# Kernel tuning notes

Measured on AMD Instinct MI355X. Metric: run time of the kernel, lower is better.

Reference implementation:

```python
import jax, jax.numpy as jnp
import numpy as np

DIM = 2048
N_HEADS = 32
HEAD_DIM = DIM // N_HEADS
D_FF = 4 * DIM
EPS = 1e-5


def layernorm(x, g, b):
    mu = jnp.mean(x, axis=-1, keepdims=True)
    var = jnp.mean(jnp.square(x - mu), axis=-1, keepdims=True)
    return (x - mu) * jax.lax.rsqrt(var + EPS) * g + b


def setup_inputs() -> dict:
    key = jax.random.key(0)
    ks = jax.random.split(key, 12)
    s = 0.02
    # Linear weights stored as [in, out] (y = x @ W + b), equivalent math to torch's x @ W.T
    return {
        "x": jax.random.normal(ks[0], (2, 2048, DIM), jnp.float32),
        "w_qkv": jax.random.normal(ks[1], (DIM, 3 * DIM), jnp.float32) * s,
        "b_qkv": jnp.zeros((3 * DIM,), jnp.float32),
        "w_o": jax.random.normal(ks[2], (DIM, DIM), jnp.float32) * s,
        "b_o": jnp.zeros((DIM,), jnp.float32),
        "g1": jnp.ones((DIM,), jnp.float32),
        "beta1": jnp.zeros((DIM,), jnp.float32),
        "w1": jax.random.normal(ks[3], (DIM, D_FF), jnp.float32) * s,
        "b1": jnp.zeros((D_FF,), jnp.float32),
        "w2": jax.random.normal(ks[4], (D_FF, DIM), jnp.float32) * s,
        "b2": jnp.zeros((DIM,), jnp.float32),
        "g2": jnp.ones((DIM,), jnp.float32),
        "beta2": jnp.zeros((DIM,), jnp.float32),
    }


def reference(x, w_qkv, b_qkv, w_o, b_o, g1, beta1, w1, b1, w2, b2, g2, beta2):
    B, T, _ = x.shape
    residual = x
    h = layernorm(x, g1, beta1)
    qkv = h @ w_qkv + b_qkv                      # [B,T,3*DIM]
    qkv = qkv.reshape(B, T, 3, N_HEADS, HEAD_DIM)
    qkv = jnp.transpose(qkv, (2, 0, 3, 1, 4))    # [3,B,H,T,D]
    q, k, v = qkv[0], qkv[1], qkv[2]
    scores = jnp.einsum("bhtd,bhsd->bhts", q, k) / np.sqrt(HEAD_DIM).astype(np.float32)
    attn = jax.nn.softmax(scores, axis=-1)       # full T x T (non-causal), as in source
    out = jnp.einsum("bhts,bhsd->bhtd", attn, v)
    out = jnp.transpose(out, (0, 2, 1, 3)).reshape(B, T, DIM)
    h = out @ w_o + b_o
    x = h + residual
    residual = x
    h = layernorm(x, g2, beta2)
    h = jax.nn.gelu(h @ w1 + b1, approximate=False)  # torch nn.GELU default = exact erf
    h = h @ w2 + b2
    return h + residual
```

## Files before the change

kernel.cpp:

```cpp
#include <hip/hip_runtime.h>
#include <hip/hip_bf16.h>

#define DIM  2048
#define DFF  8192
#define NH   32
#define HD   64
#define TT   2048
#define MM   4096

typedef __attribute__((ext_vector_type(4))) float f32x4;
typedef __attribute__((ext_vector_type(4))) unsigned int u32x4;
typedef __attribute__((ext_vector_type(2))) unsigned int u32x2;
typedef unsigned short ushort_t;

#define MFMA16(ACC, A, B) \
  asm volatile("v_mfma_f32_16x16x32_bf16 %0, %1, %2, %0" : "+v"(ACC) : "v"(A), "v"(B))
#define MFMA16A(ACC, A, B) \
  asm volatile("v_mfma_f32_16x16x32_bf16 %0, %1, %2, %0" : "+a"(ACC) : "v"(A), "v"(B))

#define GL16(GP, LP)                                                     \
  __builtin_amdgcn_global_load_lds(                                      \
      (const __attribute__((address_space(1))) void*)(GP),               \
      (__attribute__((address_space(3))) void*)(LP), 16, 0, 0)

#define VM(N) asm volatile("s_waitcnt vmcnt(" #N ")" ::: "memory")
#define NOOP  ((void)0)

template <int IMM>
__device__ __forceinline__ u32x4 dsr(unsigned a) {
  u32x4 d;
  asm volatile("ds_read_b128 %0, %1 offset:%2" : "=v"(d) : "v"(a), "i"(IMM));
  return d;
}

__device__ __forceinline__ unsigned int f2bu(float f) {
  union { __hip_bfloat16 h; unsigned short u; } c;
  c.h = __float2bfloat16(f);
  return (unsigned int)c.u;
}

__global__ __launch_bounds__(256)
void transpose_cvt(const float* __restrict__ in, __hip_bfloat16* __restrict__ out,
                   int R, int C) {
  __shared__ float tile[32][33];
  const int tx = threadIdx.x, ty = threadIdx.y;
  const int bx = blockIdx.x * 32, by = blockIdx.y * 32;
#pragma unroll
  for (int i = 0; i < 32; i += 8)
    tile[ty + i][tx] = in[(size_t)(by + ty + i) * C + bx + tx];
  __syncthreads();
#pragma unroll
  for (int i = 0; i < 32; i += 8)
    out[(size_t)(bx + ty + i) * R + by + tx] = __float2bfloat16(tile[tx][ty + i]);
}

__global__ __launch_bounds__(256)
void ln_kernel(const float* __restrict__ in, const float* __restrict__ gw,
               const float* __restrict__ bw, __hip_bfloat16* __restrict__ out) {
  const int row = blockIdx.x;
  const int t = threadIdx.x;
  const float* x = in + (size_t)row * DIM;
  const float4 v0 = ((const float4*)x)[t * 2];
  const float4 v1 = ((const float4*)x)[t * 2 + 1];
  float s  = v0.x + v0.y + v0.z + v0.w + v1.x + v1.y + v1.z + v1.w;
  float ss = v0.x*v0.x + v0.y*v0.y + v0.z*v0.z + v0.w*v0.w
           + v1.x*v1.x + v1.y*v1.y + v1.z*v1.z + v1.w*v1.w;
#pragma unroll
  for (int o = 32; o >= 1; o >>= 1) { s += __shfl_xor(s, o); ss += __shfl_xor(ss, o); }
  __shared__ float red[8];
  if ((t & 63) == 0) { red[t >> 6] = s; red[4 + (t >> 6)] = ss; }
  __syncthreads();
  s  = red[0] + red[1] + red[2] + red[3];
  ss = red[4] + red[5] + red[6] + red[7];
  const float mean = s * (1.0f / DIM);
  const float rstd = rsqrtf(ss * (1.0f / DIM) - mean * mean + 1e-5f);
  const float4 g0 = ((const float4*)gw)[t * 2], g1 = ((const float4*)gw)[t * 2 + 1];
  const float4 b0 = ((const float4*)bw)[t * 2], b1 = ((const float4*)bw)[t * 2 + 1];
  uint4 o;
  o.x = f2bu((v0.x - mean) * rstd * g0.x + b0.x) | (f2bu((v0.y - mean) * rstd * g0.y + b0.y) << 16);
  o.y = f2bu((v0.z - mean) * rstd * g0.z + b0.z) | (f2bu((v0.w - mean) * rstd * g0.w + b0.w) << 16);
  o.z = f2bu((v1.x - mean) * rstd * g1.x + b1.x) | (f2bu((v1.y - mean) * rstd * g1.y + b1.y) << 16);
  o.w = f2bu((v1.z - mean) * rstd * g1.z + b1.z) | (f2bu((v1.w - mean) * rstd * g1.w + b1.w) << 16);
  *(uint4*)((char*)out + ((size_t)row * DIM + t * 8) * 2) = o;
}

template <int EPI>
__global__ __launch_bounds__(512, 2)
void gemm256(const __hip_bfloat16* __restrict__ Abf, const __hip_bfloat16* __restrict__ Btbf,
             const float* __restrict__ bias, const float* __restrict__ res,
             void* __restrict__ o0, void* __restrict__ o1, void* __restrict__ o2,
             int M, int N, int K, int nkt) {
  __shared__ ushort_t lds[2][2][16384];
  const int tid = threadIdx.x;
  const int l = tid & 63, w = tid >> 6;
  const int wm = w >> 2, wn = w & 3;
  const int g = l >> 4, q15 = l & 15;

  const int nby = M >> 8;
  const int nwg = (N >> 8) * nby;
  int id = blockIdx.x;
  {
    const int qq = nwg >> 3, rr = nwg & 7;
    const int xcd = id & 7, pos = id >> 3;
    id = (xcd < rr ? xcd * (qq + 1) : rr * (qq + 1) + (xcd - rr) * qq) + pos;
  }
  const int bm = (id % nby) << 8;
  const int bn = (id / nby) << 8;
  const int k0 = (EPI == 4) ? (int)blockIdx.y * (nkt << 6) : 0;

  const ushort_t* Au = (const ushort_t*)Abf;
  const ushort_t* Bu = (const ushort_t*)Btbf;
  const int sr = tid >> 3;
  const int sc = (((tid & 7) ^ (sr & 7)) << 3);
  const ushort_t* aBase = Au + (size_t)(bm + sr) * K + (k0 + sc);
  const ushort_t* bBase = Bu + (size_t)(bn + sr) * K + (k0 + sc);
  const int dOff = (w << 9) + (l << 3);

#define SA(BUF, GRP, KT_)                                                \
  GL16(aBase + (size_t)((GRP) << 6) * K + ((KT_) << 6),                  \
       &lds[BUF][0][((GRP) << 12) + dOff])
#define SB(BUF, GRP, KT_)                                                \
  GL16(bBase + (size_t)((GRP) << 6) * K + ((KT_) << 6),                  \
       &lds[BUF][1][((GRP) << 12) + dOff])

  const unsigned lbase =
      (unsigned)(size_t)(__attribute__((address_space(3))) ushort_t*)&lds[0][0][0];
  const int x7 = q15 & 7;
  const unsigned laneA = (unsigned)(q15 * 128);
  const unsigned c0 = (unsigned)((g ^ x7) * 16);
  const unsigned c1 = (unsigned)(((4 | g) ^ x7) * 16);
  const unsigned aAk0b0 = lbase + wm * 8192 + laneA + c0;
  const unsigned aAk1b0 = lbase + wm * 8192 + laneA + c1;
  const unsigned aAk0b1 = aAk0b0 + 65536;
  const unsigned aAk1b1 = aAk1b0 + 65536;
  const unsigned aBk0b0 = lbase + 32768 + wn * 8192 + laneA + c0;
  const unsigned aBk1b0 = lbase + 32768 + wn * 8192 + laneA + c1;
  const unsigned aBk0b1 = aBk0b0 + 65536;
  const unsigned aBk1b1 = aBk1b0 + 65536;

#define AOFFC(M) (((M) & 4) * 4096 + ((M) & 3) * 2048)
#define RDA(BUF, M0, M1) do{                                             \
    af[0][0] = dsr<AOFFC(M0)>(aAk0b##BUF);                               \
    af[0][1] = dsr<AOFFC(M0)>(aAk1b##BUF);                               \
    af[1][0] = dsr<AOFFC(M1)>(aAk0b##BUF);                               \
    af[1][1] = dsr<AOFFC(M1)>(aAk1b##BUF); }while(0)
#define RDB(BUF) do{                                                     \
    bf[0][0] = dsr<0>(aBk0b##BUF);    bf[0][1] = dsr<0>(aBk1b##BUF);     \
    bf[1][0] = dsr<2048>(aBk0b##BUF); bf[1][1] = dsr<2048>(aBk1b##BUF);  \
    bf[2][0] = dsr<4096>(aBk0b##BUF); bf[2][1] = dsr<4096>(aBk1b##BUF);  \
    bf[3][0] = dsr<6144>(aBk0b##BUF); bf[3][1] = dsr<6144>(aBk1b##BUF); }while(0)

#define LGK0 do{ asm volatile("s_waitcnt lgkmcnt(0)" ::: "memory");      \
                 __builtin_amdgcn_sched_barrier(0); }while(0)

#define CLUSTER(R0, R1) do{                                              \
    __builtin_amdgcn_s_setprio(1);                                       \
    MFMA16A(acc[R0][0], af[0][0], bf[0][0]);                             \
    MFMA16A(acc[R0][1], af[0][0], bf[1][0]);                             \
    MFMA16A(acc[R0][2], af[0][0], bf[2][0]);                             \
    MFMA16A(acc[R0][3], af[0][0], bf[3][0]);                             \
    MFMA16A(acc[R1][0], af[1][0], bf[0][0]);                             \
    MFMA16A(acc[R1][1], af[1][0], bf[1][0]);                             \
    MFMA16A(acc[R1][2], af[1][0], bf[2][0]);                             \
    MFMA16A(acc[R1][3], af[1][0], bf[3][0]);                             \
    MFMA16A(acc[R0][0], af[0][1], bf[0][1]);                             \
    MFMA16A(acc[R0][1], af[0][1], bf[1][1]);                             \
    MFMA16A(acc[R0][2], af[0][1], bf[2][1]);                             \
    MFMA16A(acc[R0][3], af[0][1], bf[3][1]);                             \
    MFMA16A(acc[R1][0], af[1][1], bf[0][1]);                             \
    MFMA16A(acc[R1][1], af[1][1], bf[1][1]);                             \
    MFMA16A(acc[R1][2], af[1][1], bf[2][1]);                             \
    MFMA16A(acc[R1][3], af[1][1], bf[3][1]);                             \
    __builtin_amdgcn_s_setprio(0); }while(0)

#define HALF(BUF, OBUF, ktA23, PFA, ktN, PFN, W1C, W3C)                  \
  do {                                                                   \
                                               \
    if (PFA) { SA(OBUF, 2, ktA23); SA(OBUF, 3, ktA23); }                 \
    RDB(BUF); RDA(BUF, 0, 1);                                            \
    __builtin_amdgcn_s_barrier();                                        \
    LGK0; CLUSTER(0, 1);                                                 \
    __builtin_amdgcn_s_barrier();                                        \
                                                       \
    if (PFN) { SB(BUF, 0, ktN); SB(BUF, 1, ktN); }                       \
    RDA(BUF, 2, 3);                                                      \
    __builtin_amdgcn_s_barrier();                                        \
    LGK0; CLUSTER(2, 3);                                                 \
    W1C;                                                                 \
    __builtin_amdgcn_s_barrier();                                        \
                                                       \
    if (PFN) { SB(BUF, 2, ktN); SB(BUF, 3, ktN); }                       \
    RDA(BUF, 4, 5);                                                      \
    __builtin_amdgcn_s_barrier();                                        \
    LGK0; CLUSTER(4, 5);                                                 \
    __builtin_amdgcn_s_barrier();                                        \
                                                       \
    if (PFN) { SA(BUF, 0, ktN); SA(BUF, 1, ktN); }                       \
    RDA(BUF, 6, 7);                                                      \
    __builtin_amdgcn_s_barrier();                                        \
    LGK0; CLUSTER(6, 7);                                                 \
    W3C;                                                                 \
    __builtin_amdgcn_s_barrier();                                        \
  } while (0)

  f32x4 acc[8][4];
#pragma unroll
  for (int a = 0; a < 8; ++a)
#pragma unroll
    for (int b = 0; b < 4; ++b) acc[a][b] = (f32x4)0.0f;

  u32x4 bf[4][2], af[2][2];

  SB(0, 0, 0); SB(0, 1, 0); SB(0, 2, 0); SB(0, 3, 0);
  SA(0, 0, 0); SA(0, 1, 0); SA(0, 2, 0); SA(0, 3, 0);
  SB(1, 0, 1); SB(1, 1, 1); SB(1, 2, 1); SB(1, 3, 1);
  SA(1, 0, 1); SA(1, 1, 1);
  VM(8);
  __builtin_amdgcn_s_barrier();

  int kt = 0;
  for (; kt + 3 < nkt; kt += 2) {
    HALF(0, 1, kt + 1, true, kt + 2, true, VM(10), VM(8));
    HALF(1, 0, kt + 2, true, kt + 3, true, VM(10), VM(8));
  }
  HALF(0, 1, kt + 1, true,  kt + 2, false, VM(8), VM(2));
  HALF(1, 0, kt + 2, false, kt + 3, false, VM(0), NOOP);

#pragma unroll
  for (int m = 0; m < 8; ++m) {
    const int row0 = bm + ((m & 4) << 5) + (wm << 6) + ((m & 3) << 4) + (g << 2);
#pragma unroll
    for (int n = 0; n < 4; ++n) {
      const int col = bn + (wn << 6) + (n << 4) + q15;
      float bv = 0.0f;
      if constexpr (EPI != 4) bv = bias[col];
#pragma unroll
      for (int i = 0; i < 4; ++i) {
        const int mrow = row0 + i;
        float v = acc[m][n][i] + bv;
        if constexpr (EPI == 0) {
          const int sel = col >> 11, hd = col & 2047, h = hd >> 6, d = hd & 63;
          const int b = mrow >> 11, t = mrow & 2047;
          if (sel == 0) {
            ((__hip_bfloat16*)o0)[((size_t)(b * NH + h) * TT + t) * HD + d] =
                __float2bfloat16(v * 0.125f);
          } else if (sel == 1) {
            ((__hip_bfloat16*)o1)[((size_t)(b * NH + h) * TT + t) * HD + d] =
                __float2bfloat16(v);
          } else {
            ((__hip_bfloat16*)o2)[((size_t)(b * NH + h) * HD + d) * TT + t] =
                __float2bfloat16(v);
          }
        } else if constexpr (EPI == 2) {
          ((__hip_bfloat16*)o0)[(size_t)mrow * N + col] =
              __float2bfloat16(0.5f * v * (1.0f + erff(v * 0.70710678118654752f)));
        } else {
          ((float*)(blockIdx.y ? o1 : o0))[(size_t)mrow * N + col] = v;
        }
      }
    }
  }
#undef SA
#undef SB
#undef RDA
#undef RDB
#undef HALF
#undef CLUSTER
#undef LGK0
#undef AOFFC
}

__global__ __launch_bounds__(256)
void combine2(const float* __restrict__ p0, const float* __restrict__ p1,
              const float* __restrict__ bias, const float* __restrict__ res,
              float* __restrict__ out) {
  const size_t i = ((size_t)blockIdx.x * 256 + threadIdx.x) << 2;
  const float4 a = *(const float4*)(p0 + i);
  const float4 b = *(const float4*)(p1 + i);
  const float4 r = *(const float4*)(res + i);
  const float4 bi = *(const float4*)(bias + (i & (DIM - 1)));
  float4 o;
  o.x = a.x + b.x + r.x + bi.x;
  o.y = a.y + b.y + r.y + bi.y;
  o.z = a.z + b.z + r.z + bi.z;
  o.w = a.w + b.w + r.w + bi.w;
  *(float4*)(out + i) = o;
}

template <int EPI>
__global__ __launch_bounds__(256)
void gemm_bt(const __hip_bfloat16* __restrict__ A, const __hip_bfloat16* __restrict__ Bt,
             const float* __restrict__ bias, const float* __restrict__ res,
             void* __restrict__ o0, int M, int N, int K) {
  __shared__ __hip_bfloat16 As[128 * 32];
  __shared__ __hip_bfloat16 Bs[128 * 32];
  const int tid = threadIdx.x;
  const int l = tid & 63, w = tid >> 6;
  const int wr = w >> 1, wc = w & 1;
  const int g = l >> 4, q15 = l & 15;
  const int bm = blockIdx.y * 128, bn = blockIdx.x * 128;

  f32x4 acc[4][4];
#pragma unroll
  for (int a = 0; a < 4; ++a)
#pragma unroll
    for (int b = 0; b < 4; ++b) acc[a][b] = (f32x4)0.0f;

  const __hip_bfloat16* aSrc = A  + (size_t)(bm + (tid >> 2)) * K + (tid & 3) * 8;
  const __hip_bfloat16* bSrc = Bt + (size_t)(bn + (tid >> 2)) * K + (tid & 3) * 8;
  __hip_bfloat16* aDst = As + tid * 8;
  __hip_bfloat16* bDst = Bs + tid * 8;
  const size_t rowStep = (size_t)64 * K;

  for (int kt = 0; kt < K; kt += 32) {
    GL16(aSrc + kt,            aDst);
    GL16(aSrc + rowStep + kt,  aDst + 2048);
    GL16(bSrc + kt,            bDst);
    GL16(bSrc + rowStep + kt,  bDst + 2048);
    __syncthreads();
    u32x4 af[4], bf[4];
#pragma unroll
    for (int rb = 0; rb < 4; ++rb)
      af[rb] = *(const u32x4*)(As + (wr * 64 + rb * 16 + q15) * 32 + g * 8);
#pragma unroll
    for (int cb = 0; cb < 4; ++cb)
      bf[cb] = *(const u32x4*)(Bs + (wc * 64 + cb * 16 + q15) * 32 + g * 8);
#pragma unroll
    for (int rb = 0; rb < 4; ++rb)
#pragma unroll
      for (int cb = 0; cb < 4; ++cb) MFMA16(acc[rb][cb], af[rb], bf[cb]);
    __syncthreads();
  }

#pragma unroll
  for (int rb = 0; rb < 4; ++rb) {
    const int row0 = bm + wr * 64 + rb * 16 + g * 4;
#pragma unroll
    for (int cb = 0; cb < 4; ++cb) {
      const int col = bn + wc * 64 + cb * 16 + q15;
      const float bv = bias[col];
#pragma unroll
      for (int i = 0; i < 4; ++i) {
        const int m = row0 + i;
        float v = acc[rb][cb][i] + bv;
        ((float*)o0)[(size_t)m * N + col] = v + res[(size_t)m * N + col];
      }
    }
  }
}

__global__ __launch_bounds__(256)
void attn_kernel(const __hip_bfloat16* __restrict__ Q, const __hip_bfloat16* __restrict__ Kx,
                 const __hip_bfloat16* __restrict__ Vt, __hip_bfloat16* __restrict__ out) {
  __shared__ unsigned int Plds[4][2048];
  const int tid = threadIdx.x;
  const int l = tid & 63, w = tid >> 6;
  const int g = l >> 4, q15 = l & 15;
  const int bh = blockIdx.x >> 3;
  const int q0 = (blockIdx.x & 7) * 256 + w * 64;
  const __hip_bfloat16* Qb = Q  + (size_t)bh * TT * HD;
  const __hip_bfloat16* Kb = Kx + (size_t)bh * TT * HD;
  const __hip_bfloat16* Vb = Vt + (size_t)bh * HD * TT;
  unsigned int* Pw = Plds[w];

  u32x4 qf[4][2];
#pragma unroll
  for (int rb = 0; rb < 4; ++rb)
#pragma unroll
    for (int ks = 0; ks < 2; ++ks)
      qf[rb][ks] = *(const u32x4*)(Qb + (size_t)(q0 + rb * 16 + q15) * HD + ks * 32 + g * 8);

  f32x4 acc[4][4];
#pragma unroll
  for (int a = 0; a < 4; ++a)
#pragma unroll
    for (int b = 0; b < 4; ++b) acc[a][b] = (f32x4)0.0f;
  float mstat[4] = {-3e38f, -3e38f, -3e38f, -3e38f};
  float lstat[4] = {0.f, 0.f, 0.f, 0.f};

  for (int s0 = 0; s0 < TT; s0 += 64) {
    f32x4 st[4][4];
#pragma unroll
    for (int a = 0; a < 4; ++a)
#pragma unroll
      for (int b = 0; b < 4; ++b) st[a][b] = (f32x4)0.0f;
#pragma unroll
    for (int ks = 0; ks < 2; ++ks) {
      u32x4 kf[4];
#pragma unroll
      for (int cb = 0; cb < 4; ++cb)
        kf[cb] = *(const u32x4*)(Kb + (size_t)(s0 + cb * 16 + q15) * HD + ks * 32 + g * 8);
#pragma unroll
      for (int cb = 0; cb < 4; ++cb)
#pragma unroll
        for (int rb = 0; rb < 4; ++rb) MFMA16(st[cb][rb], kf[cb], qf[rb][ks]);
    }
#pragma unroll
    for (int rb = 0; rb < 4; ++rb) {
      float pm = st[0][rb][0];
#pragma unroll
      for (int cb = 0; cb < 4; ++cb)
#pragma unroll
        for (int i = 0; i < 4; ++i) pm = fmaxf(pm, st[cb][rb][i]);
      pm = fmaxf(pm, __shfl_xor(pm, 16));
      pm = fmaxf(pm, __shfl_xor(pm, 32));
      const float mnew = fmaxf(mstat[rb], pm);
      const float corr = __expf(mstat[rb] - mnew);
      mstat[rb] = mnew;
      float rs = 0.f;
#pragma unroll
      for (int cb = 0; cb < 4; ++cb)
#pragma unroll
        for (int i = 0; i < 4; ++i) {
          const float p = __expf(st[cb][rb][i] - mnew);
          st[cb][rb][i] = p;
          rs += p;
        }
      rs += __shfl_xor(rs, 16);
      rs += __shfl_xor(rs, 32);
      lstat[rb] = lstat[rb] * corr + rs;
#pragma unroll
      for (int db = 0; db < 4; ++db)
#pragma unroll
        for (int i = 0; i < 4; ++i) acc[db][rb][i] *= corr;
      const int row = rb * 16 + q15;
      const int rx = row & 7;
#pragma unroll
      for (int cb = 0; cb < 4; ++cb) {
        const unsigned int lo = f2bu(st[cb][rb][0]) | (f2bu(st[cb][rb][1]) << 16);
        const unsigned int hi = f2bu(st[cb][rb][2]) | (f2bu(st[cb][rb][3]) << 16);
        const int seg = (cb * 2 + (g >> 1)) ^ rx;
        u32x2 pk = {lo, hi};
        *(u32x2*)(Pw + row * 32 + seg * 4 + (g & 1) * 2) = pk;
      }
    }
#pragma unroll
    for (int ks2 = 0; ks2 < 2; ++ks2) {
      u32x4 vf[4], pf[4];
#pragma unroll
      for (int db = 0; db < 4; ++db)
        vf[db] = *(const u32x4*)(Vb + (size_t)(db * 16 + q15) * TT + s0 + ks2 * 32 + g * 8);
#pragma unroll
      for (int rb = 0; rb < 4; ++rb) {
        const int row = rb * 16 + q15;
        const int seg = (ks2 * 4 + g) ^ (row & 7);
        pf[rb] = *(const u32x4*)(Pw + row * 32 + seg * 4);
      }
#pragma unroll
      for (int db = 0; db < 4; ++db)
#pragma unroll
        for (int rb = 0; rb < 4; ++rb) MFMA16(acc[db][rb], vf[db], pf[rb]);
    }
  }
  const int b = bh >> 5, hh = bh & 31;
#pragma unroll
  for (int rb = 0; rb < 4; ++rb) {
    const float inv = 1.0f / lstat[rb];
    const size_t trow = (size_t)(b * TT + q0 + rb * 16 + q15);
#pragma unroll
    for (int db = 0; db < 4; ++db) {
      const unsigned int lo = f2bu(acc[db][rb][0] * inv) | (f2bu(acc[db][rb][1] * inv) << 16);
      const unsigned int hi = f2bu(acc[db][rb][2] * inv) | (f2bu(acc[db][rb][3] * inv) << 16);
      u32x2 pk = {lo, hi};
      *(u32x2*)(out + trow * DIM + hh * 64 + db * 16 + g * 4) = pk;
    }
  }
}

extern "C" void kernel_launch(void* const* d_in, const int* in_sizes, int n_in,
                              void* d_out, int out_size, void* d_ws, size_t ws_size,
                              hipStream_t stream) {
  (void)in_sizes; (void)n_in; (void)out_size; (void)ws_size;
  const float* x     = (const float*)d_in[0];
  const float* w_qkv = (const float*)d_in[1];
  const float* b_qkv = (const float*)d_in[2];
  const float* w_o   = (const float*)d_in[3];
  const float* b_o   = (const float*)d_in[4];
  const float* g1    = (const float*)d_in[5];
  const float* be1   = (const float*)d_in[6];
  const float* w1    = (const float*)d_in[7];
  const float* b1    = (const float*)d_in[8];
  const float* w2    = (const float*)d_in[9];
  const float* b2    = (const float*)d_in[10];
  const float* g2    = (const float*)d_in[11];
  const float* be2   = (const float*)d_in[12];

  char* ws = (char*)d_ws;
  size_t off = 0;
  auto alloc = [&](size_t bytes) {
    void* p = ws + off;
    off += (bytes + 255) & ~(size_t)255;
    return p;
  };
  __hip_bfloat16* WqkvT = (__hip_bfloat16*)alloc((size_t)6144 * 2048 * 2);
  __hip_bfloat16* WoT   = (__hip_bfloat16*)alloc((size_t)2048 * 2048 * 2);
  __hip_bfloat16* W1T   = (__hip_bfloat16*)alloc((size_t)8192 * 2048 * 2);
  __hip_bfloat16* W2T   = (__hip_bfloat16*)alloc((size_t)2048 * 8192 * 2);
  __hip_bfloat16* hbuf  = (__hip_bfloat16*)alloc((size_t)MM * DIM * 2);
  float*          xres  = (float*)alloc((size_t)MM * DIM * 4);
  __hip_bfloat16* Qb    = (__hip_bfloat16*)alloc((size_t)MM * DIM * 2);
  __hip_bfloat16* Kb    = (__hip_bfloat16*)alloc((size_t)MM * DIM * 2);
  __hip_bfloat16* Vtb   = (__hip_bfloat16*)alloc((size_t)MM * DIM * 2);
  __hip_bfloat16* attno = (__hip_bfloat16*)alloc((size_t)MM * DIM * 2);
  __hip_bfloat16* f1    = Qb;
  float* p0 = (float*)ws;
  float* p1 = (float*)(ws + (size_t)MM * DIM * 4);

  const dim3 tb(32, 8);
  transpose_cvt<<<dim3(6144 / 32, 2048 / 32), tb, 0, stream>>>(w_qkv, WqkvT, 2048, 6144);
  transpose_cvt<<<dim3(2048 / 32, 2048 / 32), tb, 0, stream>>>(w_o, WoT, 2048, 2048);
  transpose_cvt<<<dim3(8192 / 32, 2048 / 32), tb, 0, stream>>>(w1, W1T, 2048, 8192);
  transpose_cvt<<<dim3(2048 / 32, 8192 / 32), tb, 0, stream>>>(w2, W2T, 8192, 2048);

  ln_kernel<<<MM, 256, 0, stream>>>(x, g1, be1, hbuf);
  gemm256<0><<<dim3((6144 / 256) * (MM / 256)), 512, 0, stream>>>(
      hbuf, WqkvT, b_qkv, nullptr, Qb, Kb, Vtb, MM, 6144, 2048, 32);
  attn_kernel<<<512, 256, 0, stream>>>(Qb, Kb, Vtb, attno);
  gemm_bt<1><<<dim3(2048 / 128, MM / 128), 256, 0, stream>>>(
      attno, WoT, b_o, x, xres, MM, 2048, 2048);
  ln_kernel<<<MM, 256, 0, stream>>>(xres, g2, be2, hbuf);
  gemm256<2><<<dim3((8192 / 256) * (MM / 256)), 512, 0, stream>>>(
      hbuf, W1T, b1, nullptr, f1, nullptr, nullptr, MM, 8192, 2048, 32);
  gemm256<4><<<dim3((2048 / 256) * (MM / 256), 2), 512, 0, stream>>>(
      f1, W2T, nullptr, nullptr, p0, p1, nullptr, MM, 2048, 8192, 64);
  combine2<<<(MM * DIM) / 1024, 256, 0, stream>>>(p0, p1, b2, xres, (float*)d_out);
}
```

Before: 757.2 us.

## Speed up attention softmax with exp2, lazy rescale, K prefetch and packed converts

Folds log2(e) into the Q scale so the softmax can use the raw v_exp_f32 (base-2) instruction. It also skips the running-max rescale of the accumulator unless the new max exceeds the old by more than a threshold, and uses max3 reductions and packed bf16 conversion. K fragments are prefetched one tile ahead into registers, and MFMA blocks are wrapped with setprio. Each of these removes VALU work or load latency from the attention inner loop. The costs are more register pressure and the lazy rescale letting exponentials reach up to 2^8 before renormalising.

```diff
diff --git a/kernel.cpp b/kernel.cpp
--- a/kernel.cpp
+++ b/kernel.cpp
@@ -37,6 +37,17 @@
   union { __hip_bfloat16 h; unsigned short u; } c;
   c.h = __float2bfloat16(f);
   return (unsigned int)c.u;
+}
+__device__ __forceinline__ float fexp2(float x) {
+  float r; asm("v_exp_f32 %0, %1" : "=v"(r) : "v"(x)); return r;
+}
+__device__ __forceinline__ unsigned cvtpk(float lo, float hi) {
+  unsigned r; asm("v_cvt_pk_bf16_f32 %0, %1, %2" : "=v"(r) : "v"(lo), "v"(hi));
+  return r;
+}
+__device__ __forceinline__ float fmax3(float a, float b, float c) {
+  float r; asm("v_max3_f32 %0, %1, %2, %3" : "=v"(r) : "v"(a), "v"(b), "v"(c));
+  return r;
 }
 
 __global__ __launch_bounds__(256)
@@ -175,26 +186,22 @@
 
 #define HALF(BUF, OBUF, ktA23, PFA, ktN, PFN, W1C, W3C)                  \
   do {                                                                   \
-                                               \
     if (PFA) { SA(OBUF, 2, ktA23); SA(OBUF, 3, ktA23); }                 \
     RDB(BUF); RDA(BUF, 0, 1);                                            \
     __builtin_amdgcn_s_barrier();                                        \
     LGK0; CLUSTER(0, 1);                                                 \
     __builtin_amdgcn_s_barrier();                                        \
-                                                       \
     if (PFN) { SB(BUF, 0, ktN); SB(BUF, 1, ktN); }                       \
     RDA(BUF, 2, 3);                                                      \
     __builtin_amdgcn_s_barrier();                                        \
     LGK0; CLUSTER(2, 3);                                                 \
     W1C;                                                                 \
     __builtin_amdgcn_s_barrier();                                        \
-                                                       \
     if (PFN) { SB(BUF, 2, ktN); SB(BUF, 3, ktN); }                       \
     RDA(BUF, 4, 5);                                                      \
     __builtin_amdgcn_s_barrier();                                        \
     LGK0; CLUSTER(4, 5);                                                 \
     __builtin_amdgcn_s_barrier();                                        \
-                                                       \
     if (PFN) { SA(BUF, 0, ktN); SA(BUF, 1, ktN); }                       \
     RDA(BUF, 6, 7);                                                      \
     __builtin_amdgcn_s_barrier();                                        \
@@ -243,7 +250,7 @@
           const int b = mrow >> 11, t = mrow & 2047;
           if (sel == 0) {
             ((__hip_bfloat16*)o0)[((size_t)(b * NH + h) * TT + t) * HD + d] =
-                __float2bfloat16(v * 0.125f);
+                __float2bfloat16(v * 0.18033688011112042f);
           } else if (sel == 1) {
             ((__hip_bfloat16*)o1)[((size_t)(b * NH + h) * TT + t) * HD + d] =
                 __float2bfloat16(v);
@@ -378,79 +385,96 @@
   float mstat[4] = {-3e38f, -3e38f, -3e38f, -3e38f};
   float lstat[4] = {0.f, 0.f, 0.f, 0.f};
 
+  u32x4 kf[2][4];
+#pragma unroll
+  for (int cb = 0; cb < 4; ++cb)
+#pragma unroll
+    for (int ks = 0; ks < 2; ++ks)
+      kf[ks][cb] = *(const u32x4*)(Kb + (size_t)(cb * 16 + q15) * HD + ks * 32 + g * 8);
+
   for (int s0 = 0; s0 < TT; s0 += 64) {
     f32x4 st[4][4];
 #pragma unroll
     for (int a = 0; a < 4; ++a)
 #pragma unroll
       for (int b = 0; b < 4; ++b) st[a][b] = (f32x4)0.0f;
-#pragma unroll
-    for (int ks = 0; ks < 2; ++ks) {
-      u32x4 kf[4];
+    __builtin_amdgcn_s_setprio(1);
+#pragma unroll
+    for (int ks = 0; ks < 2; ++ks)
 #pragma unroll
       for (int cb = 0; cb < 4; ++cb)
-        kf[cb] = *(const u32x4*)(Kb + (size_t)(s0 + cb * 16 + q15) * HD + ks * 32 + g * 8);
+#pragma unroll
+        for (int rb = 0; rb < 4; ++rb) MFMA16(st[cb][rb], kf[ks][cb], qf[rb][ks]);
+    __builtin_amdgcn_s_setprio(0);
+    if (s0 + 64 < TT) {
 #pragma unroll
       for (int cb = 0; cb < 4; ++cb)
 #pragma unroll
-        for (int rb = 0; rb < 4; ++rb) MFMA16(st[cb][rb], kf[cb], qf[rb][ks]);
+        for (int ks = 0; ks < 2; ++ks)
+          kf[ks][cb] = *(const u32x4*)(Kb + (size_t)(s0 + 64 + cb * 16 + q15) * HD + ks * 32 + g * 8);
     }
 #pragma unroll
     for (int rb = 0; rb < 4; ++rb) {
-      float pm = st[0][rb][0];
-#pragma unroll
-      for (int cb = 0; cb < 4; ++cb)
-#pragma unroll
-        for (int i = 0; i < 4; ++i) pm = fmaxf(pm, st[cb][rb][i]);
+      float a0 = fmax3(st[0][rb][0], st[0][rb][1], st[0][rb][2]);
+      float a1 = fmax3(st[0][rb][3], st[1][rb][0], st[1][rb][1]);
+      float a2 = fmax3(st[1][rb][2], st[1][rb][3], st[2][rb][0]);
+      float a3 = fmax3(st[2][rb][1], st[2][rb][2], st[2][rb][3]);
+      float a4 = fmax3(st[3][rb][0], st[3][rb][1], st[3][rb][2]);
+      float pm = fmax3(fmax3(a0, a1, a2), a3, fmax3(a4, st[3][rb][3], a0));
       pm = fmaxf(pm, __shfl_xor(pm, 16));
       pm = fmaxf(pm, __shfl_xor(pm, 32));
-      const float mnew = fmaxf(mstat[rb], pm);
-      const float corr = __expf(mstat[rb] - mnew);
-      mstat[rb] = mnew;
+      if (!__all(pm <= mstat[rb] + 8.0f)) {
+        const float mnew = fmaxf(mstat[rb], pm);
+        const float corr = fexp2(mstat[rb] - mnew);
+        mstat[rb] = mnew;
+        lstat[rb] *= corr;
+#pragma unroll
+        for (int db = 0; db < 4; ++db)
+#pragma unroll
+          for (int i = 0; i < 4; ++i) acc[db][rb][i] *= corr;
+      }
+      const float mcur = mstat[rb];
       float rs = 0.f;
-#pragma unroll
-      for (int cb = 0; cb < 4; ++cb)
-#pragma unroll
-        for (int i = 0; i < 4; ++i) {
-          const float p = __expf(st[cb][rb][i] - mnew);
-          st[cb][rb][i] = p;
-          rs += p;
-        }
+      const int row = rb * 16 + q15;
+      const int rx = row & 7;
+#pragma unroll
+      for (int cb = 0; cb < 4; ++cb) {
+        const float p0 = fexp2(st[cb][rb][0] - mcur);
+        const float p1 = fexp2(st[cb][rb][1] - mcur);
+        const float p2 = fexp2(st[cb][rb][2] - mcur);
+        const float p3 = fexp2(st[cb][rb][3] - mcur);
+        rs += (p0 + p1) + (p2 + p3);
+        const int seg = (cb * 2 + (g >> 1)) ^ rx;
+        u32x2 pk = {cvtpk(p0, p1), cvtpk(p2, p3)};
+        *(u32x2*)(Pw + row * 32 + seg * 4 + (g & 1) * 2) = pk;
+      }
       rs += __shfl_xor(rs, 16);
       rs += __shfl_xor(rs, 32);
-      lstat[rb] = lstat[rb] * corr + rs;
+      lstat[rb] += rs;
+    }
+    u32x4 vf[2][4];
+#pragma unroll
+    for (int ks2 = 0; ks2 < 2; ++ks2)
 #pragma unroll
       for (int db = 0; db < 4; ++db)
-#pragma unroll
-        for (int i = 0; i < 4; ++i) acc[db][rb][i] *= corr;
-      const int row = rb * 16 + q15;
-      const int rx = row & 7;
-#pragma unroll
-      for (int cb = 0; cb < 4; ++cb) {
-        const unsigned int lo = f2bu(st[cb][rb][0]) | (f2bu(st[cb][rb][1]) << 16);
-        const unsigned int hi = f2bu(st[cb][rb][2]) | (f2bu(st[cb][rb][3]) << 16);
-        const int seg = (cb * 2 + (g >> 1)) ^ rx;
-        u32x2 pk = {lo, hi};
-        *(u32x2*)(Pw + row * 32 + seg * 4 + (g & 1) * 2) = pk;
-      }
-    }
-#pragma unroll
-    for (int ks2 = 0; ks2 < 2; ++ks2) {
-      u32x4 vf[4], pf[4];
-#pragma unroll
-      for (int db = 0; db < 4; ++db)
-        vf[db] = *(const u32x4*)(Vb + (size_t)(db * 16 + q15) * TT + s0 + ks2 * 32 + g * 8);
+        vf[ks2][db] = *(const u32x4*)(Vb + (size_t)(db * 16 + q15) * TT + s0 + ks2 * 32 + g * 8);
+    u32x4 pf[2][4];
+#pragma unroll
+    for (int ks2 = 0; ks2 < 2; ++ks2)
 #pragma unroll
       for (int rb = 0; rb < 4; ++rb) {
         const int row = rb * 16 + q15;
         const int seg = (ks2 * 4 + g) ^ (row & 7);
-        pf[rb] = *(const u32x4*)(Pw + row * 32 + seg * 4);
+        pf[ks2][rb] = *(const u32x4*)(Pw + row * 32 + seg * 4);
       }
+    __builtin_amdgcn_s_setprio(1);
+#pragma unroll
+    for (int ks2 = 0; ks2 < 2; ++ks2)
 #pragma unroll
       for (int db = 0; db < 4; ++db)
 #pragma unroll
-        for (int rb = 0; rb < 4; ++rb) MFMA16(acc[db][rb], vf[db], pf[rb]);
-    }
+        for (int rb = 0; rb < 4; ++rb) MFMA16(acc[db][rb], vf[ks2][db], pf[ks2][rb]);
+    __builtin_amdgcn_s_setprio(0);
   }
   const int b = bh >> 5, hh = bh & 31;
 #pragma unroll
@@ -459,9 +483,8 @@
     const size_t trow = (size_t)(b * TT + q0 + rb * 16 + q15);
 #pragma unroll
     for (int db = 0; db < 4; ++db) {
-      const unsigned int lo = f2bu(acc[db][rb][0] * inv) | (f2bu(acc[db][rb][1] * inv) << 16);
-      const unsigned int hi = f2bu(acc[db][rb][2] * inv) | (f2bu(acc[db][rb][3] * inv) << 16);
-      u32x2 pk = {lo, hi};
+      u32x2 pk = {cvtpk(acc[db][rb][0] * inv, acc[db][rb][1] * inv),
+                  cvtpk(acc[db][rb][2] * inv, acc[db][rb][3] * inv)};
       *(u32x2*)(out + trow * DIM + hh * 64 + db * 16 + g * 4) = pk;
     }
   }
```

After: 718.1 us. -5.2%, faster.
